# Performance work log

Measured on AMD Instinct MI355X. Metric: run time of the kernel, lower is better.

Reference implementation:

```python
import jax, jax.numpy as jnp
import numpy as np

EPS = 1e-12

def layernorm(x, g, b):
    m = jnp.mean(x, axis=-1, keepdims=True)
    v = jnp.mean((x - m) ** 2, axis=-1, keepdims=True)
    return (x - m) * jax.lax.rsqrt(v + EPS) * g + b

def setup_inputs() -> dict:
    key = jax.random.key(0)
    ks = jax.random.split(key, 12)
    B, S, H, D, M = 64, 512, 768, 16, 50
    std = 0.02
    return {
        "hidden_states": jax.random.normal(ks[0], (B, S, H), dtype=jnp.float32),
        "g1": jnp.ones((H,), jnp.float32), "b1": jnp.zeros((H,), jnp.float32),
        "W_down": jax.random.normal(ks[1], (H, D), jnp.float32) * std,
        "b_down": jnp.zeros((D,), jnp.float32),
        "g2": jnp.ones((D,), jnp.float32), "b2": jnp.zeros((D,), jnp.float32),
        "memory": jax.random.normal(ks[2], (M, D), jnp.float32) * std,
        "W_k": jax.random.normal(ks[3], (D, D), jnp.float32) * std,
        "b_k": jnp.zeros((D,), jnp.float32),
        "W_v": jax.random.normal(ks[4], (D, D), jnp.float32) * std,
        "b_v": jnp.zeros((D,), jnp.float32),
        "g3": jnp.ones((D,), jnp.float32), "b3": jnp.zeros((D,), jnp.float32),
        "W_up": jax.random.normal(ks[5], (D, H), jnp.float32) * std,
        "b_up": jnp.zeros((H,), jnp.float32),
        "layer_id": 0,
    }

def reference(hidden_states, g1, b1, W_down, b_down, g2, b2, memory, W_k, b_k, W_v, b_v, g3, b3, W_up, b_up, layer_id):
    # ln_1 -> down_project -> ln_2 -> MemoryNet -> ln_3 -> up_project (no residual in memory branch)
    h = layernorm(hidden_states, g1, b1)                 # [B,S,H]
    d = h @ W_down + b_down                              # [B,S,D]
    q = layernorm(d, g2, b2)                             # [B,S,D]
    key = memory @ W_k + b_k                             # [M,D]
    val = memory @ W_v + b_v                             # [M,D]
    score = jax.nn.softmax(jnp.einsum('bsd,md->bsm', q, key), axis=-1)  # [B,S,M]
    mem_out = jnp.einsum('bsm,md->bsd', score, val)      # [B,S,D]
    mem_out = layernorm(mem_out, g3, b3)
    return mem_out @ W_up + b_up                         # [B,S,H]
```

## Files before the change

### kernel.cpp

```cpp
#include <hip/hip_runtime.h>
#include <cstdint>

#define LN_EPS 1e-12f
#define NTOK 32768
#define HDIM 768
#define DDIM 16
#define MMEM 50

#define WS_G    0
#define WS_C    16
#define WS_KEY  32
#define WS_VAL  832
#define WS_WT   1632

typedef short bf16x8 __attribute__((ext_vector_type(8)));
typedef float f32x4 __attribute__((ext_vector_type(4)));

__device__ __forceinline__ unsigned f2bf(float f) {
    const unsigned u = __builtin_bit_cast(unsigned, f);
    return (u + 0x7FFFu + ((u >> 16) & 1u)) >> 16;
}

__global__ __launch_bounds__(256) void pre_kernel(
    const float* __restrict__ g1, const float* __restrict__ b1,
    const float* __restrict__ W_down, const float* __restrict__ b_down,
    const float* __restrict__ memory, const float* __restrict__ W_k,
    const float* __restrict__ b_k, const float* __restrict__ W_v,
    const float* __restrict__ b_v, float* __restrict__ ws)
{
    const int tid = threadIdx.x;
    const int blk = blockIdx.x;
    if (blk > 0) {
        const int e0 = (blk - 1) * 1024 + tid * 4;
        const int n  = e0 / HDIM;
        const int h  = e0 - n * HDIM;
        const unsigned r0 = f2bf(g1[h+0]*W_down[(h+0)*DDIM+n])
                          | (f2bf(g1[h+1]*W_down[(h+1)*DDIM+n]) << 16);
        const unsigned r1 = f2bf(g1[h+2]*W_down[(h+2)*DDIM+n])
                          | (f2bf(g1[h+3]*W_down[(h+3)*DDIM+n]) << 16);
        *(uint2*)((unsigned short*)(ws + WS_WT) + e0) = make_uint2(r0, r1);
        return;
    }
    __shared__ float redG[16][17];
    __shared__ float redC[16][17];
    const int k = tid & 15, g = tid >> 4;
    float pG = 0.f, pC = 0.f;
    for (int i = g*(HDIM/16); i < (g+1)*(HDIM/16); ++i) {
        const float w = W_down[i*DDIM + k];
        pG = fmaf(g1[i], w, pG);
        pC = fmaf(b1[i], w, pC);
    }
    redG[g][k] = pG; redC[g][k] = pC;
    __syncthreads();
    if (tid < 16) {
        float sG = 0.f, sC = 0.f;
        for (int gg = 0; gg < 16; ++gg) { sG += redG[gg][tid]; sC += redC[gg][tid]; }
        ws[WS_G + tid] = sG;
        ws[WS_C + tid] = sC + b_down[tid];
    }
    for (int e = tid; e < MMEM*DDIM; e += 256) {
        const int m = e >> 4, kk = e & 15;
        float sk = b_k[kk], sv = b_v[kk];
        for (int dd = 0; dd < DDIM; ++dd) {
            const float mv = memory[m*DDIM + dd];
            sk = fmaf(mv, W_k[dd*DDIM + kk], sk);
            sv = fmaf(mv, W_v[dd*DDIM + kk], sv);
        }
        ws[WS_KEY + e] = sk;
        ws[WS_VAL + e] = sv;
    }
}

#define LOADCHUNK(CC, RR)                                                     \
    {                                                                         \
        _Pragma("unroll")                                                     \
        for (int j = 0; j < 4; ++j)                                           \
            (RR)[j] = *(const float4*)(x + (size_t)(tok0 + lr)*HDIM           \
                                       + (hbase + (CC))*64 + j*16 + lc*4);    \
    }

#define CVTWRITE(RR)                                                          \
    {                                                                         \
        _Pragma("unroll")                                                     \
        for (int j = 0; j < 4; ++j) {                                         \
            const float4 v = (RR)[j];                                         \
            s0 += v.x + v.y + v.z + v.w;                                      \
            s1 = fmaf(v.x,v.x,fmaf(v.y,v.y,fmaf(v.z,v.z,fmaf(v.w,v.w,s1)))); \
            const unsigned ux = __builtin_bit_cast(unsigned, v.x);            \
            const unsigned uy = __builtin_bit_cast(unsigned, v.y);            \
            const unsigned uz = __builtin_bit_cast(unsigned, v.z);            \
            const unsigned uw = __builtin_bit_cast(unsigned, v.w);            \
            const unsigned h01 = (ux >> 16) | (uy & 0xFFFF0000u);             \
            const unsigned h23 = (uz >> 16) | (uw & 0xFFFF0000u);             \
            const int col4 = j*4 + lc;                                        \
            const int gg   = col4 >> 1;                                       \
            const int off_ = wbase + lr*128 + ((gg ^ (lr & 7)))*16            \
                           + (col4 & 1)*8;                                    \
            *(uint2*)(lds + off_) = make_uint2(h01, h23);                     \
        }                                                                     \
    }

__global__ __launch_bounds__(256) void fused_kernel(
    const float* __restrict__ x, const float* __restrict__ ws,
    const float* __restrict__ g2, const float* __restrict__ b2,
    const float* __restrict__ g3, const float* __restrict__ b3,
    const float* __restrict__ W_up, const float* __restrict__ b_up,
    float* __restrict__ out)
{
    __shared__ __align__(16) char lds[30208];
    const int tid  = threadIdx.x;
    const int lane = tid & 63;
    const int w    = tid >> 6;
    const int p    = w >> 1;
    const int sb   = w & 1;
    const int wbase = w * 4096;
    const int hbase = sb * 6;
    const int t0   = blockIdx.x * 32;
    const int tok0 = t0 + p * 16;

    const int lr = lane >> 2;
    const int lc = lane & 3;

    float s0 = 0.f, s1 = 0.f;
    float4 ldr[2][4];

    LOADCHUNK(0, ldr[0])
    LOADCHUNK(1, ldr[1])

    float* KV = (float*)(lds + 16384);
    {
        const float4* src = (const float4*)(ws + WS_KEY);
        float4* dst = (float4*)KV;
        dst[tid] = src[tid];
        if (tid < 144) dst[256 + tid] = src[256 + tid];
    }

    CVTWRITE(ldr[0])

    f32x4 acc = {0.f, 0.f, 0.f, 0.f};
    const int fr   = lane & 15;
    const int frx7 = fr & 7;
    const int fq   = lane >> 4;
    const unsigned short* __restrict__ WTg =
        (const unsigned short*)(ws + WS_WT) + (lane & 15)*768 + fq*8;

#pragma unroll
    for (int hc = 0; hc < 6; ++hc) {
        if (hc + 2 < 6) LOADCHUNK(hc + 2, ldr[hc & 1])
#pragma unroll
        for (int kk = 0; kk < 2; ++kk) {
            const int gx = kk*4 + fq;
            const bf16x8 ah = *(const bf16x8*)(lds + wbase + fr*128
                                               + ((gx ^ frx7))*16);
            const bf16x8 bw = *(const bf16x8*)(WTg + (hbase + hc)*64 + kk*32);
            acc = __builtin_amdgcn_mfma_f32_16x16x32_bf16(bw, ah, acc, 0, 0, 0);
        }
        if (hc + 1 < 6) CVTWRITE(ldr[(hc + 1) & 1])
    }

    float* trans = (float*)(lds + 22784);
    float* trp = trans + (p*2 + sb)*304;
#pragma unroll
    for (int i = 0; i < 4; ++i)
        trp[fr*19 + fq*4 + i] = acc[i];
    s0 += __shfl_xor(s0, 1, 64); s0 += __shfl_xor(s0, 2, 64);
    s1 += __shfl_xor(s1, 1, 64); s1 += __shfl_xor(s1, 2, 64);
    if (lc == 0) { trp[lr*19 + 16] = s0; trp[lr*19 + 17] = s1; }

    __syncthreads();

    const int sg = lane >> 4;
    const int tw = fr;
    const float* trA = trans + (p*2 + 0)*304;
    const float* trB = trans + (p*2 + 1)*304;
    float fA[16];
#pragma unroll
    for (int k = 0; k < 16; ++k) fA[k] = trA[tw*19 + k] + trB[tw*19 + k];
    const float fS0 = trA[tw*19 + 16] + trB[tw*19 + 16];
    const float fS1 = trA[tw*19 + 17] + trB[tw*19 + 17];

    const float inv_h = 1.0f / 768.0f;
    const float mean1 = fS0 * inv_h;
    const float var1 = fmaf(-mean1, mean1, fS1 * inv_h);
    const float rs1 = rsqrtf(var1 + LN_EPS);
    float d[16];
#pragma unroll
    for (int k = 0; k < 16; ++k)
        d[k] = fmaf(rs1, fmaf(-mean1, ws[WS_G + k], fA[k]), ws[WS_C + k]);

    float t0s = 0.f;
#pragma unroll
    for (int k = 0; k < 16; ++k) t0s += d[k];
    const float mean2 = t0s * 0.0625f;
    float t1s = 0.f;
#pragma unroll
    for (int k = 0; k < 16; ++k) { const float c = d[k] - mean2; t1s = fmaf(c, c, t1s); }
    const float rs2 = rsqrtf(t1s * 0.0625f + LN_EPS);
    float qv[16];
#pragma unroll
    for (int k = 0; k < 16; ++k)
        qv[k] = fmaf((d[k] - mean2) * rs2, g2[k], b2[k]);

    const int mm0 = (sg < 2) ? sg*13 : 26 + (sg - 2)*12;
    const int mm1 = mm0 + ((sg < 2) ? 13 : 12);
    float mo[16];
#pragma unroll
    for (int k = 0; k < 16; ++k) mo[k] = 0.f;
    float ssum = 0.f;
#pragma unroll 1
    for (int mm = mm0; mm < mm1; ++mm) {
        float a = 0.f;
#pragma unroll
        for (int k = 0; k < 16; ++k) a = fmaf(qv[k], KV[mm*16 + k], a);
        const float e = __expf(a);
        ssum += e;
#pragma unroll
        for (int k = 0; k < 16; ++k) mo[k] = fmaf(e, KV[800 + mm*16 + k], mo[k]);
    }
    ssum += __shfl_xor(ssum, 16, 64);
    ssum += __shfl_xor(ssum, 32, 64);
#pragma unroll
    for (int k = 0; k < 16; ++k) {
        mo[k] += __shfl_xor(mo[k], 16, 64);
        mo[k] += __shfl_xor(mo[k], 32, 64);
    }
    const float rn = 1.0f / ssum;
#pragma unroll
    for (int k = 0; k < 16; ++k) mo[k] *= rn;

    float u0 = 0.f;
#pragma unroll
    for (int k = 0; k < 16; ++k) u0 += mo[k];
    const float mean3 = u0 * 0.0625f;
    float u1 = 0.f;
#pragma unroll
    for (int k = 0; k < 16; ++k) { const float c = mo[k] - mean3; u1 = fmaf(c, c, u1); }
    const float rs3 = rsqrtf(u1 * 0.0625f + LN_EPS);

    float4 mq;
    if (sg == 0)      mq = make_float4(mo[0],  mo[1],  mo[2],  mo[3]);
    else if (sg == 1) mq = make_float4(mo[4],  mo[5],  mo[6],  mo[7]);
    else if (sg == 2) mq = make_float4(mo[8],  mo[9],  mo[10], mo[11]);
    else              mq = make_float4(mo[12], mo[13], mo[14], mo[15]);
    const float4 gq = *(const float4*)(g3 + sg*4);
    const float4 bq = *(const float4*)(b3 + sg*4);
    float4 stv;
    stv.x = fmaf((mq.x - mean3) * rs3, gq.x, bq.x);
    stv.y = fmaf((mq.y - mean3) * rs3, gq.y, bq.y);
    stv.z = fmaf((mq.z - mean3) * rs3, gq.z, bq.z);
    stv.w = fmaf((mq.w - mean3) * rs3, gq.w, bq.w);

    float* r_lds = (float*)(lds + 27648) + p*320;
    *(float4*)(r_lds + tw*20 + sg*4) = stv;

#pragma unroll 1
    for (int jg = 0; jg < 3; ++jg) {
        const int j0 = jg * 256 + lane * 4;
        float4 wv[16];
#pragma unroll
        for (int k = 0; k < 16; ++k)
            wv[k] = *(const float4*)(W_up + k*HDIM + j0);
        const float4 bu = *(const float4*)(b_up + j0);
#pragma unroll 2
        for (int tt = 0; tt < 8; ++tt) {
            const int tloc = sb*8 + tt;
            const float* rt = r_lds + tloc*20;
            float4 a2 = bu;
#pragma unroll
            for (int k = 0; k < 16; ++k) {
                const float rk = rt[k];
                a2.x = fmaf(rk, wv[k].x, a2.x);
                a2.y = fmaf(rk, wv[k].y, a2.y);
                a2.z = fmaf(rk, wv[k].z, a2.z);
                a2.w = fmaf(rk, wv[k].w, a2.w);
            }
            f32x4 sv = { a2.x, a2.y, a2.z, a2.w };
            __builtin_nontemporal_store(sv,
                (f32x4*)(out + (size_t)(tok0 + tloc) * HDIM + j0));
        }
    }
}

extern "C" void kernel_launch(void* const* d_in, const int* in_sizes, int n_in,
                              void* d_out, int out_size, void* d_ws, size_t ws_size,
                              hipStream_t stream) {
    const float* x      = (const float*)d_in[0];
    const float* g1     = (const float*)d_in[1];
    const float* b1     = (const float*)d_in[2];
    const float* W_down = (const float*)d_in[3];
    const float* b_down = (const float*)d_in[4];
    const float* g2     = (const float*)d_in[5];
    const float* b2     = (const float*)d_in[6];
    const float* memory = (const float*)d_in[7];
    const float* W_k    = (const float*)d_in[8];
    const float* b_k    = (const float*)d_in[9];
    const float* W_v    = (const float*)d_in[10];
    const float* b_v    = (const float*)d_in[11];
    const float* g3     = (const float*)d_in[12];
    const float* b3     = (const float*)d_in[13];
    const float* W_up   = (const float*)d_in[14];
    const float* b_up   = (const float*)d_in[15];
    float* out = (float*)d_out;
    float* ws  = (float*)d_ws;

    hipLaunchKernelGGL(pre_kernel, dim3(13), dim3(256), 0, stream,
                       g1, b1, W_down, b_down, memory, W_k, b_k, W_v, b_v, ws);
    hipLaunchKernelGGL(fused_kernel, dim3(NTOK/32), dim3(256), 0, stream,
                       x, ws, g2, b2, g3, b3, W_up, b_up, out);
}
```

Baseline: 42.00 us.

## Split each token tile's hidden-dim reduction across four waves instead of two

```diff
diff --git a/kernel.cpp b/kernel.cpp
--- a/kernel.cpp
+++ b/kernel.cpp
@@ -100,21 +100,21 @@
         }                                                                     \
     }
 
-__global__ __launch_bounds__(256) void fused_kernel(
+__global__ __launch_bounds__(512) void fused_kernel(
     const float* __restrict__ x, const float* __restrict__ ws,
     const float* __restrict__ g2, const float* __restrict__ b2,
     const float* __restrict__ g3, const float* __restrict__ b3,
     const float* __restrict__ W_up, const float* __restrict__ b_up,
     float* __restrict__ out)
 {
-    __shared__ __align__(16) char lds[30208];
+    __shared__ __align__(16) char lds[35072];
     const int tid  = threadIdx.x;
     const int lane = tid & 63;
     const int w    = tid >> 6;
-    const int p    = w >> 1;
-    const int sb   = w & 1;
-    const int wbase = w * 4096;
-    const int hbase = sb * 6;
+    const int p    = w >> 2;
+    const int sq   = w & 3;
+    const int wbase = w * 2048;
+    const int hbase = sq * 3;
     const int t0   = blockIdx.x * 32;
     const int tok0 = t0 + p * 16;
 
@@ -131,8 +131,7 @@
     {
         const float4* src = (const float4*)(ws + WS_KEY);
         float4* dst = (float4*)KV;
-        dst[tid] = src[tid];
-        if (tid < 144) dst[256 + tid] = src[256 + tid];
+        if (tid < 400) dst[tid] = src[tid];
     }
 
     CVTWRITE(ldr[0])
@@ -145,8 +144,8 @@
         (const unsigned short*)(ws + WS_WT) + (lane & 15)*768 + fq*8;
 
 #pragma unroll
-    for (int hc = 0; hc < 6; ++hc) {
-        if (hc + 2 < 6) LOADCHUNK(hc + 2, ldr[hc & 1])
+    for (int hc = 0; hc < 3; ++hc) {
+        if (hc + 2 < 3) LOADCHUNK(hc + 2, ldr[hc & 1])
 #pragma unroll
         for (int kk = 0; kk < 2; ++kk) {
             const int gx = kk*4 + fq;
@@ -155,11 +154,11 @@
             const bf16x8 bw = *(const bf16x8*)(WTg + (hbase + hc)*64 + kk*32);
             acc = __builtin_amdgcn_mfma_f32_16x16x32_bf16(bw, ah, acc, 0, 0, 0);
         }
-        if (hc + 1 < 6) CVTWRITE(ldr[(hc + 1) & 1])
+        if (hc + 1 < 3) CVTWRITE(ldr[(hc + 1) & 1])
     }
 
     float* trans = (float*)(lds + 22784);
-    float* trp = trans + (p*2 + sb)*304;
+    float* trp = trans + w*304;
 #pragma unroll
     for (int i = 0; i < 4; ++i)
         trp[fr*19 + fq*4 + i] = acc[i];
@@ -171,13 +170,18 @@
 
     const int sg = lane >> 4;
     const int tw = fr;
-    const float* trA = trans + (p*2 + 0)*304;
-    const float* trB = trans + (p*2 + 1)*304;
     float fA[16];
-#pragma unroll
-    for (int k = 0; k < 16; ++k) fA[k] = trA[tw*19 + k] + trB[tw*19 + k];
-    const float fS0 = trA[tw*19 + 16] + trB[tw*19 + 16];
-    const float fS1 = trA[tw*19 + 17] + trB[tw*19 + 17];
+    float fS0 = 0.f, fS1 = 0.f;
+#pragma unroll
+    for (int k = 0; k < 16; ++k) fA[k] = 0.f;
+#pragma unroll
+    for (int s = 0; s < 4; ++s) {
+        const float* trs = trans + (p*4 + s)*304;
+#pragma unroll
+        for (int k = 0; k < 16; ++k) fA[k] += trs[tw*19 + k];
+        fS0 += trs[tw*19 + 16];
+        fS1 += trs[tw*19 + 17];
+    }
 
     const float inv_h = 1.0f / 768.0f;
     const float mean1 = fS0 * inv_h;
@@ -250,7 +254,7 @@
     stv.z = fmaf((mq.z - mean3) * rs3, gq.z, bq.z);
     stv.w = fmaf((mq.w - mean3) * rs3, gq.w, bq.w);
 
-    float* r_lds = (float*)(lds + 27648) + p*320;
+    float* r_lds = (float*)(lds + 32512) + p*320;
     *(float4*)(r_lds + tw*20 + sg*4) = stv;
 
 #pragma unroll 1
@@ -262,9 +266,9 @@
             wv[k] = *(const float4*)(W_up + k*HDIM + j0);
         const float4 bu = *(const float4*)(b_up + j0);
 #pragma unroll 2
-        for (int tt = 0; tt < 8; ++tt) {
-            const int tloc = sb*8 + tt;
-            const float* rt = r_lds + tloc*20;
+        for (int tt = 0; tt < 4; ++tt) {
+            const int tg = sq*4 + tt;
+            const float* rt = r_lds + tg*20;
             float4 a2 = bu;
 #pragma unroll
             for (int k = 0; k < 16; ++k) {
@@ -276,7 +280,7 @@
             }
             f32x4 sv = { a2.x, a2.y, a2.z, a2.w };
             __builtin_nontemporal_store(sv,
-                (f32x4*)(out + (size_t)(tok0 + tloc) * HDIM + j0));
+                (f32x4*)(out + (size_t)(tok0 + tg) * HDIM + j0));
         }
     }
 }
@@ -305,6 +309,6 @@
 
     hipLaunchKernelGGL(pre_kernel, dim3(13), dim3(256), 0, stream,
                        g1, b1, W_down, b_down, memory, W_k, b_k, W_v, b_v, ws);
-    hipLaunchKernelGGL(fused_kernel, dim3(NTOK/32), dim3(256), 0, stream,
+    hipLaunchKernelGGL(fused_kernel, dim3(NTOK/32), dim3(512), 0, stream,
                        x, ws, g2, b2, g3, b3, W_up, b_up, out);
 }
```

Result: slower. 55.71 us (+32.6%).
